# Kernel optimization log

Measured on AMD Instinct MI355X. Metric: run time of the kernel, lower is better.

Reference implementation:

```python
import jax, jax.numpy as jnp
import numpy as np

N_NODES = 10000
N_EDGES = 100000
C = 64          # in_channels == out_channels (required by x_i + x_m)
D_EDGE = 16     # edge_attr feature dim


def setup_inputs() -> dict:
    key = jax.random.key(0)
    k_x, k_ei, k_ea, k_w, k_b, k_r, k_bias = jax.random.split(key, 7)
    x = jax.random.normal(k_x, (N_NODES, C), dtype=jnp.float32)
    edge_index = jax.random.randint(k_ei, (2, N_EDGES), 0, N_NODES, dtype=jnp.int32)
    edge_attr = jax.random.normal(k_ea, (N_EDGES, D_EDGE), dtype=jnp.float32)
    # nn = Linear(D_EDGE -> C*C), producing per-edge [C, C] weight matrices
    W_nn = jax.random.normal(k_w, (D_EDGE, C * C), dtype=jnp.float32) * (1.0 / np.sqrt(D_EDGE))
    b_nn = jax.random.normal(k_b, (C * C,), dtype=jnp.float32) * 0.01
    root = jax.random.normal(k_r, (C, C), dtype=jnp.float32) * (1.0 / np.sqrt(C))
    bias = jax.random.normal(k_bias, (C,), dtype=jnp.float32) * 0.01
    return {"x": x, "edge_index": edge_index, "edge_attr": edge_attr,
            "W_nn": W_nn, "b_nn": b_nn, "root": root, "bias": bias}


def reference(x, edge_index, edge_attr, W_nn, b_nn, root, bias):
    N, Cc = x.shape
    row, col = edge_index[0], edge_index[1]
    # per-edge weight matrices from nn(edge_attr): [E, C, C]
    e = (edge_attr @ W_nn + b_nn).reshape(-1, Cc, Cc)
    # gather source features and apply edge-conditioned matmul: [E, C]
    m = jnp.einsum('ec,eco->eo', x[row], e)
    # Faithful to torch loop: x_m[i] = m[col == i].mean() -> SCALAR mean over
    # all elements of incoming messages, broadcast across the feature row.
    seg_sum = jax.ops.segment_sum(m.sum(axis=1), col, num_segments=N)       # [N]
    cnt = jax.ops.segment_sum(jnp.ones_like(col, dtype=x.dtype), col,
                              num_segments=N) * Cc                            # [N]
    mean = jnp.where(cnt > 0, seg_sum / jnp.maximum(cnt, 1.0), 0.0)          # [N]
    x_m = jnp.broadcast_to(mean[:, None], (N, Cc))                            # [N, C]
    # root transform + bias
    out = x @ root + bias + x_m
    return out
```

## Files before the change

### kernel.cpp

```cpp
#include <hip/hip_runtime.h>
#include <hip/hip_bf16.h>


#define CC 64
#define DE 16
#define PAD 65

__global__ __launch_bounds__(256) void k_edge_direct(const float* __restrict__ W,
                                                     const float* __restrict__ b,
                                                     const float* __restrict__ x,
                                                     const int* __restrict__ ei,
                                                     const float* __restrict__ ea,
                                                     float* __restrict__ seg,
                                                     float* __restrict__ cnt,
                                                     int E) {
    __shared__ float ws[1024 + CC];
    const int tid = threadIdx.x;

    for (int p = tid; p < 1024 + CC; p += 256) {
        const float4* src = (p < 1024) ? (const float4*)(W + (size_t)p * CC)
                                       : (const float4*)(b + (size_t)(p - 1024) * CC);
        float s = 0.f;
#pragma unroll
        for (int i = 0; i < 16; ++i) { float4 v = src[i]; s += v.x + v.y + v.z + v.w; }
        ws[p] = s;
    }
    __syncthreads();

    int e = blockIdx.x * 256 + tid;
    if (e >= E) return;

    const int r  = ei[e];
    const int cn = ei[E + e];

    const float4* a4 = (const float4*)(ea + (size_t)e * DE);
    float4 av[4];
#pragma unroll
    for (int i = 0; i < 4; ++i) av[i] = a4[i];
    float eas[DE] = { av[0].x, av[0].y, av[0].z, av[0].w,
                      av[1].x, av[1].y, av[1].z, av[1].w,
                      av[2].x, av[2].y, av[2].z, av[2].w,
                      av[3].x, av[3].y, av[3].z, av[3].w };

    const float4* ws4 = (const float4*)ws;
    const float4* bs4 = (const float4*)(ws + 1024);
    float4 u[16];
#pragma unroll
    for (int c4 = 0; c4 < 16; ++c4) u[c4] = bs4[c4];
#pragma unroll
    for (int d = 0; d < DE; ++d) {
        float ed = eas[d];
#pragma unroll
        for (int c4 = 0; c4 < 16; ++c4) {
            float4 w = ws4[d * 16 + c4];
            u[c4].x += ed * w.x; u[c4].y += ed * w.y;
            u[c4].z += ed * w.z; u[c4].w += ed * w.w;
        }
    }

    const float4* x4 = (const float4*)(x + (size_t)r * CC);
    float s = 0.f;
#pragma unroll
    for (int c4 = 0; c4 < 16; ++c4) {
        float4 xv = x4[c4];
        s += u[c4].x * xv.x + u[c4].y * xv.y + u[c4].z * xv.z + u[c4].w * xv.w;
    }

    atomicAdd(seg + cn, s);
    atomicAdd(cnt + cn, 1.0f);
}

__global__ __launch_bounds__(256) void k_final(const float* __restrict__ x,
                                               const float* __restrict__ root,
                                               const float* __restrict__ bias,
                                               const float* __restrict__ seg,
                                               const float* __restrict__ cnt,
                                               float* __restrict__ out,
                                               int N) {
    __shared__ float rt[CC * CC];
    __shared__ float xs[16 * PAD];
    __shared__ float bi[CC];
    __shared__ float mn[16];
    int tid = threadIdx.x;
    int n0 = blockIdx.x * 16;

#pragma unroll
    for (int i = 0; i < 16; ++i) rt[tid + i * 256] = root[tid + i * 256];
#pragma unroll
    for (int it = 0; it < 4; ++it) {
        int i = it * 256 + tid;
        if ((size_t)n0 * CC + i < (size_t)N * CC)
            xs[(i >> 6) * PAD + (i & 63)] = x[(size_t)n0 * CC + i];
    }
    if (tid < CC) bi[tid] = bias[tid];
    if (tid < 16 && n0 + tid < N) {
        float c = cnt[n0 + tid];
        mn[tid] = c > 0.f ? seg[n0 + tid] / (c * (float)CC) : 0.f;
    }
    __syncthreads();

    int nl = tid >> 4, ci = tid & 15;
    int n = n0 + nl;
    if (n >= N) return;

    const float4* rt4 = (const float4*)rt;
    const float4* bi4 = (const float4*)bi;
    float m = mn[nl];
    float4 bv = bi4[ci];
    float4 acc = make_float4(bv.x + m, bv.y + m, bv.z + m, bv.w + m);
#pragma unroll
    for (int k = 0; k < CC; ++k) {
        float a  = xs[nl * PAD + k];
        float4 w = rt4[k * 16 + ci];
        acc.x += a * w.x; acc.y += a * w.y; acc.z += a * w.z; acc.w += a * w.w;
    }
    *(float4*)(out + (size_t)n * CC + ci * 4) = acc;
}

extern "C" void kernel_launch(void* const* d_in, const int* in_sizes, int n_in,
                              void* d_out, int out_size, void* d_ws, size_t ws_size,
                              hipStream_t stream) {
    const float* x    = (const float*)d_in[0];
    const int*   ei   = (const int*)  d_in[1];
    const float* ea   = (const float*)d_in[2];
    const float* W    = (const float*)d_in[3];
    const float* b    = (const float*)d_in[4];
    const float* root = (const float*)d_in[5];
    const float* bias = (const float*)d_in[6];
    float* out = (float*)d_out;
    float* ws  = (float*)d_ws;

    const int N = in_sizes[0] / CC;
    const int E = in_sizes[1] / 2;

    float* seg = ws;
    float* cnt = ws + N;

    int eBlocks = (E + 255) / 256;
    int fBlocks = (N + 15) / 16;

    k_edge_direct<<<eBlocks, 256, 0, stream>>>(W, b, x, ei, ea, seg, cnt, E);
    k_final      <<<fBlocks, 256, 0, stream>>>(x, root, bias, seg, cnt, out, N);
}
```

Measured before the change: 104.8 us.

## Replace global atomics with per-edge scores and block-local LDS segment reduction

The edge kernel now writes one scalar score per edge instead of atomically adding into global per-node sums and counts. A second kernel with 64 blocks owns a contiguous slice of nodes. Each block scans the full destination-index array and accumulates matching scores and counts with shared-memory atomics, then runs the root GEMM tile by tile for its slice. This removes global atomic contention and the dependence on a pre-zeroed workspace. The cost is that every block rereads all edge indices and scores, and only 64 blocks do the final GEMM, which leaves most of the GPU idle.

```diff
diff --git a/kernel.cpp b/kernel.cpp
--- a/kernel.cpp
+++ b/kernel.cpp
@@ -5,33 +5,33 @@
 #define CC 64
 #define DE 16
 #define PAD 65
+#define NB2 64
+#define SLMAX 160
 
-__global__ __launch_bounds__(256) void k_edge_direct(const float* __restrict__ W,
-                                                     const float* __restrict__ b,
-                                                     const float* __restrict__ x,
-                                                     const int* __restrict__ ei,
-                                                     const float* __restrict__ ea,
-                                                     float* __restrict__ seg,
-                                                     float* __restrict__ cnt,
-                                                     int E) {
+__global__ __launch_bounds__(256) void k_score(const float* __restrict__ W,
+                                               const float* __restrict__ b,
+                                               const float* __restrict__ x,
+                                               const int* __restrict__ ei,
+                                               const float* __restrict__ ea,
+                                               float* __restrict__ s,
+                                               int E) {
     __shared__ float ws[1024 + CC];
     const int tid = threadIdx.x;
 
     for (int p = tid; p < 1024 + CC; p += 256) {
         const float4* src = (p < 1024) ? (const float4*)(W + (size_t)p * CC)
                                        : (const float4*)(b + (size_t)(p - 1024) * CC);
-        float s = 0.f;
+        float v = 0.f;
 #pragma unroll
-        for (int i = 0; i < 16; ++i) { float4 v = src[i]; s += v.x + v.y + v.z + v.w; }
-        ws[p] = s;
+        for (int i = 0; i < 16; ++i) { float4 q = src[i]; v += q.x + q.y + q.z + q.w; }
+        ws[p] = v;
     }
     __syncthreads();
 
     int e = blockIdx.x * 256 + tid;
     if (e >= E) return;
 
-    const int r  = ei[e];
-    const int cn = ei[E + e];
+    const int r = ei[e];
 
     const float4* a4 = (const float4*)(ea + (size_t)e * DE);
     float4 av[4];
@@ -59,62 +59,86 @@
     }
 
     const float4* x4 = (const float4*)(x + (size_t)r * CC);
-    float s = 0.f;
+    float acc = 0.f;
 #pragma unroll
     for (int c4 = 0; c4 < 16; ++c4) {
         float4 xv = x4[c4];
-        s += u[c4].x * xv.x + u[c4].y * xv.y + u[c4].z * xv.z + u[c4].w * xv.w;
+        acc += u[c4].x * xv.x + u[c4].y * xv.y + u[c4].z * xv.z + u[c4].w * xv.w;
     }
-
-    atomicAdd(seg + cn, s);
-    atomicAdd(cnt + cn, 1.0f);
+    s[e] = acc;
 }
 
-__global__ __launch_bounds__(256) void k_final(const float* __restrict__ x,
-                                               const float* __restrict__ root,
-                                               const float* __restrict__ bias,
-                                               const float* __restrict__ seg,
-                                               const float* __restrict__ cnt,
-                                               float* __restrict__ out,
-                                               int N) {
+__global__ __launch_bounds__(256) void k_reduce_gemm(const float* __restrict__ x,
+                                                     const float* __restrict__ root,
+                                                     const float* __restrict__ bias,
+                                                     const int* __restrict__ ei,
+                                                     const float* __restrict__ s,
+                                                     float* __restrict__ out,
+                                                     int N, int E, int SL) {
     __shared__ float rt[CC * CC];
     __shared__ float xs[16 * PAD];
     __shared__ float bi[CC];
+    __shared__ float segs[SLMAX];
+    __shared__ float cnts[SLMAX];
     __shared__ float mn[16];
-    int tid = threadIdx.x;
-    int n0 = blockIdx.x * 16;
+    const int tid = threadIdx.x;
+    const int n0 = blockIdx.x * SL;
 
-#pragma unroll
-    for (int i = 0; i < 16; ++i) rt[tid + i * 256] = root[tid + i * 256];
-#pragma unroll
-    for (int it = 0; it < 4; ++it) {
-        int i = it * 256 + tid;
-        if ((size_t)n0 * CC + i < (size_t)N * CC)
-            xs[(i >> 6) * PAD + (i & 63)] = x[(size_t)n0 * CC + i];
-    }
+    for (int i = tid; i < CC * CC; i += 256) rt[i] = root[i];
     if (tid < CC) bi[tid] = bias[tid];
-    if (tid < 16 && n0 + tid < N) {
-        float c = cnt[n0 + tid];
-        mn[tid] = c > 0.f ? seg[n0 + tid] / (c * (float)CC) : 0.f;
+    for (int i = tid; i < SL; i += 256) { segs[i] = 0.f; cnts[i] = 0.f; }
+    __syncthreads();
+
+    const int* __restrict__ col = ei + E;
+#pragma unroll 4
+    for (int e = tid; e < E; e += 256) {
+        int c = col[e];
+        unsigned l = (unsigned)(c - n0);
+        if (l < (unsigned)SL) {
+            atomicAdd(&segs[l], s[e]);
+            atomicAdd(&cnts[l], 1.0f);
+        }
     }
     __syncthreads();
 
-    int nl = tid >> 4, ci = tid & 15;
-    int n = n0 + nl;
-    if (n >= N) return;
-
+    const int nl = tid >> 4, ci = tid & 15;
     const float4* rt4 = (const float4*)rt;
     const float4* bi4 = (const float4*)bi;
-    float m = mn[nl];
-    float4 bv = bi4[ci];
-    float4 acc = make_float4(bv.x + m, bv.y + m, bv.z + m, bv.w + m);
+    const int tiles = (SL + 15) >> 4;
+
+    for (int t = 0; t < tiles; ++t) {
+        int base = n0 + t * 16;
+        __syncthreads();
 #pragma unroll
-    for (int k = 0; k < CC; ++k) {
-        float a  = xs[nl * PAD + k];
-        float4 w = rt4[k * 16 + ci];
-        acc.x += a * w.x; acc.y += a * w.y; acc.z += a * w.z; acc.w += a * w.w;
+        for (int j = 0; j < 4; ++j) {
+            int i = j * 256 + tid;
+            int rrow = t * 16 + (i >> 6);
+            if (rrow < SL && (size_t)base * CC + i < (size_t)N * CC)
+                xs[(i >> 6) * PAD + (i & 63)] = x[(size_t)base * CC + i];
+        }
+        if (tid < 16) {
+            int l = t * 16 + tid, n = base + tid;
+            if (l < SL && n < N) {
+                float c = cnts[l];
+                mn[tid] = c > 0.5f ? segs[l] / (c * (float)CC) : 0.f;
+            }
+        }
+        __syncthreads();
+        int l = t * 16 + nl, n = base + nl;
+        if (l < SL && n < N) {
+            float m = mn[nl];
+            float4 bv = bi4[ci];
+            float4 acc = make_float4(bv.x + m, bv.y + m, bv.z + m, bv.w + m);
+#pragma unroll
+            for (int k = 0; k < CC; ++k) {
+                float a  = xs[nl * PAD + k];
+                float4 w = rt4[k * 16 + ci];
+                acc.x += a * w.x; acc.y += a * w.y;
+                acc.z += a * w.z; acc.w += a * w.w;
+            }
+            *(float4*)(out + (size_t)n * CC + ci * 4) = acc;
+        }
     }
-    *(float4*)(out + (size_t)n * CC + ci * 4) = acc;
 }
 
 extern "C" void kernel_launch(void* const* d_in, const int* in_sizes, int n_in,
@@ -133,12 +157,11 @@
     const int N = in_sizes[0] / CC;
     const int E = in_sizes[1] / 2;
 
-    float* seg = ws;
-    float* cnt = ws + N;
+    float* s = ws;
 
+    const int SL = (N + NB2 - 1) / NB2;
     int eBlocks = (E + 255) / 256;
-    int fBlocks = (N + 15) / 16;
 
-    k_edge_direct<<<eBlocks, 256, 0, stream>>>(W, b, x, ei, ea, seg, cnt, E);
-    k_final      <<<fBlocks, 256, 0, stream>>>(x, root, bias, seg, cnt, out, N);
+    k_score      <<<eBlocks, 256, 0, stream>>>(W, b, x, ei, ea, s, E);
+    k_reduce_gemm<<<NB2,     256, 0, stream>>>(x, root, bias, ei, s, out, N, E, SL);
 }
```

Result: slower. 243.5 us (+132.3%).
